# Kernel optimization log

Measured on AMD Instinct MI355X. Metric: run time of the kernel, lower is better.

The kernel has to match this reference:

```python
import jax, jax.numpy as jnp
import numpy as np

DIM = 1024
HEADS = 16
HEAD_DIM = DIM // HEADS
SCALE = HEAD_DIM ** -0.5


def setup_inputs() -> dict:
    key = jax.random.key(0)
    k1, k2, k3, k4 = jax.random.split(key, 4)
    x = jax.random.normal(k1, (8, 1024, DIM), dtype=jnp.float32)
    # nn.Linear weight is [out, in]; init ~ small values
    W_qkv = jax.random.normal(k2, (3 * DIM, DIM), dtype=jnp.float32) * 0.02
    W_proj = jax.random.normal(k3, (DIM, DIM), dtype=jnp.float32) * 0.02
    b_proj = jax.random.normal(k4, (DIM,), dtype=jnp.float32) * 0.02
    return {"x": x, "W_qkv": W_qkv, "W_proj": W_proj, "b_proj": b_proj}


def reference(x, W_qkv, W_proj, b_proj):
    b, n, _ = x.shape
    h, d = HEADS, HEAD_DIM
    qkv = x @ W_qkv.T  # [b, n, 3*dim]
    # rearrange 'b n (qkv h d) -> qkv b h n d'
    qkv = qkv.reshape(b, n, 3, h, d).transpose(2, 0, 3, 1, 4)
    q, k, v = qkv[0], qkv[1], qkv[2]  # each [b, h, n, d]
    dots = jnp.einsum('bhid,bhjd->bhij', q, k) * SCALE
    attn = jax.nn.softmax(dots, axis=-1)
    out = jnp.einsum('bhij,bhjd->bhid', attn, v)
    out = out.transpose(0, 2, 1, 3).reshape(b, n, h * d)  # b n (h d)
    return out @ W_proj.T + b_proj
```

## Files before the change

kernel.cpp:

```cpp
#include <hip/hip_runtime.h>
#include <math.h>

#define DIM   1024
#define HEADS 16
#define HDIM  64
#define SEQ   1024
#define BATCH 8
#define QSCALE 0.1803368801111204f
#define LDH   72
#define ABM   128

typedef __attribute__((ext_vector_type(8))) short          short8_t;
typedef __attribute__((ext_vector_type(8))) unsigned short ushort8_t;
typedef __attribute__((ext_vector_type(4))) unsigned short ushort4_t;
typedef __attribute__((ext_vector_type(4))) float          floatx4;

__device__ __forceinline__ unsigned short f2bf(float f) {
    unsigned u = __float_as_uint(f);
    u += 0x7fffu + ((u >> 16) & 1u);
    return (unsigned short)(u >> 16);
}
__device__ __forceinline__ unsigned rnd_bf(float f) {
    unsigned u = __float_as_uint(f);
    return u + 0x7fffu + ((u >> 16) & 1u);
}
__device__ __forceinline__ float fast_exp2(float x) {
#if __has_builtin(__builtin_amdgcn_exp2f)
    return __builtin_amdgcn_exp2f(x);
#else
    return exp2f(x);
#endif
}
__device__ __forceinline__ void glds16(const unsigned short* g, unsigned short* l) {
    __builtin_amdgcn_global_load_lds(
        (const __attribute__((address_space(1))) void*)g,
        (__attribute__((address_space(3))) void*)l, 16, 0, 0);
}

__global__ __launch_bounds__(256) void cvt_bf16_all(const float* __restrict__ x,
                                                    const float* __restrict__ wqkv,
                                                    const float* __restrict__ wproj,
                                                    unsigned short* __restrict__ x_o,
                                                    unsigned short* __restrict__ wqkv_o,
                                                    unsigned short* __restrict__ wproj_o) {
    const int N8_X = BATCH * SEQ * DIM / 8;
    const int N8_WQ = 3 * DIM * DIM / 8;
    const int N8_WP = DIM * DIM / 8;
    int i = blockIdx.x * 256 + threadIdx.x;
    const float* in;
    unsigned short* out;
    if (i < N8_X)               { in = x;     out = x_o; }
    else if (i < N8_X + N8_WQ)  { i -= N8_X;  in = wqkv; out = wqkv_o; }
    else                        { i -= N8_X + N8_WQ;
                                  if (i >= N8_WP) return;
                                  in = wproj; out = wproj_o; }
    const float4* p = (const float4*)in + (size_t)i * 2;
    float4 a = p[0], b = p[1];
    ushort8_t u;
    u[0] = f2bf(a.x); u[1] = f2bf(a.y); u[2] = f2bf(a.z); u[3] = f2bf(a.w);
    u[4] = f2bf(b.x); u[5] = f2bf(b.y); u[6] = f2bf(b.z); u[7] = f2bf(b.w);
    ((ushort8_t*)out)[i] = u;
}

template<int MODE>
__global__ __launch_bounds__(256) void gemm_nt_mfma(const unsigned short* __restrict__ A,
                                                    const unsigned short* __restrict__ B,
                                                    const float* __restrict__ bias,
                                                    void* __restrict__ Cout,
                                                    unsigned short* __restrict__ vt,
                                                    int M, int N, int K) {
    __shared__ __align__(16) unsigned short As[128 * 64];
    __shared__ __align__(16) unsigned short Bs[128 * 64];

    const int tid  = threadIdx.x;
    const int lane = tid & 63;
    const int wave = tid >> 6;
    const int wm = (wave >> 1) * 64;
    const int wn = (wave & 1) * 64;
    const size_t brow = (size_t)blockIdx.y * 128;
    const size_t bcol = (size_t)blockIdx.x * 128;

    const int srow   = lane >> 3;
    const int schunk = (lane & 7) ^ srow;
    const unsigned short* gA = A + (brow + wave * 8 + srow) * (size_t)K + schunk * 8;
    const unsigned short* gB = B + (bcol + wave * 8 + srow) * (size_t)K + schunk * 8;
    unsigned short* lA = &As[wave * 512 + lane * 8];
    unsigned short* lB = &Bs[wave * 512 + lane * 8];

    floatx4 acc[4][4];
    #pragma unroll
    for (int i = 0; i < 4; i++)
        #pragma unroll
        for (int j = 0; j < 4; j++) acc[i][j] = (floatx4){0.f, 0.f, 0.f, 0.f};

    const int g  = lane >> 4;
    const int rr = lane & 15;
    const int xr = rr & 7;

    for (int k0 = 0; k0 < K; k0 += 64) {
        __syncthreads();
        #pragma unroll
        for (int r = 0; r < 4; r++) {
            glds16(gA + (size_t)r * 32 * K + k0, lA + r * 2048);
            glds16(gB + (size_t)r * 32 * K + k0, lB + r * 2048);
        }
        __syncthreads();

        #pragma unroll
        for (int kc = 0; kc < 2; kc++) {
            const int ch = ((kc * 4 + g) ^ xr) * 8;
            short8_t af[4], bfr[4];
            #pragma unroll
            for (int mi = 0; mi < 4; mi++)
                af[mi] = *(const short8_t*)&As[(wm + mi * 16 + rr) * 64 + ch];
            #pragma unroll
            for (int ni = 0; ni < 4; ni++)
                bfr[ni] = *(const short8_t*)&Bs[(wn + ni * 16 + rr) * 64 + ch];
            #pragma unroll
            for (int mi = 0; mi < 4; mi++)
                #pragma unroll
                for (int ni = 0; ni < 4; ni++)
                    acc[mi][ni] = __builtin_amdgcn_mfma_f32_16x16x32_bf16(
                        af[mi], bfr[ni], acc[mi][ni], 0, 0, 0);
        }
    }

    const int crow = (lane >> 4) * 4;
    const int ccol = lane & 15;

    if (MODE == 0) {
        #pragma unroll
        for (int mi = 0; mi < 4; mi++)
            #pragma unroll
            for (int ni = 0; ni < 4; ni++) {
                const size_t col = bcol + wn + ni * 16 + ccol;
                const float bv = bias[col];
                #pragma unroll
                for (int r = 0; r < 4; r++) {
                    const size_t row = brow + wm + mi * 16 + crow + r;
                    ((float*)Cout)[row * N + col] = acc[mi][ni][r] + bv;
                }
            }
    } else {
        if (bcol < 2048) {
            const float sc = (bcol < 1024) ? QSCALE : 1.0f;
            unsigned short* qk = (unsigned short*)Cout;
            #pragma unroll
            for (int mi = 0; mi < 4; mi++)
                #pragma unroll
                for (int ni = 0; ni < 4; ni++) {
                    const size_t col = bcol + wn + ni * 16 + ccol;
                    #pragma unroll
                    for (int r = 0; r < 4; r++) {
                        const size_t row = brow + wm + mi * 16 + crow + r;
                        qk[row * 2048 + col] = f2bf(acc[mi][ni][r] * sc);
                    }
                }
        } else {
            #pragma unroll
            for (int mi = 0; mi < 4; mi++)
                #pragma unroll
                for (int ni = 0; ni < 4; ni++) {
                    const int dall = (int)(bcol + wn + ni * 16 + ccol) - 2048;
                    const int h = dall >> 6, d = dall & 63;
                    const size_t row0 = brow + wm + mi * 16 + crow;
                    const size_t bb = row0 >> 10;
                    const int n0 = (int)(row0 & 1023);
                    ushort4_t o;
                    #pragma unroll
                    for (int r = 0; r < 4; r++) o[r] = f2bf(acc[mi][ni][r]);
                    *(ushort4_t*)&vt[(((size_t)bb * HEADS + h) * HDIM + d) * SEQ + n0] = o;
                }
        }
    }
}

__global__ __launch_bounds__(256) void attn_mfma(const unsigned short* __restrict__ qk,
                                                 const unsigned short* __restrict__ vt,
                                                 unsigned short* __restrict__ aout) {
    const int qt = blockIdx.x;
    const int h  = blockIdx.y;
    const int b  = blockIdx.z;
    const int tid  = threadIdx.x;
    const int lane = tid & 63;
    const int wave = tid >> 6;
    const int g = lane >> 4;
    const int c = lane & 15;

    __shared__ __align__(16) unsigned short Qs[ABM * LDH];
    __shared__ __align__(16) unsigned short Ks[64 * LDH];
    __shared__ __align__(16) unsigned short Vs[64 * LDH];
    __shared__ float scr[4][2][16];

    const int sr = tid >> 2;
    const int sq = tid & 3;
    const unsigned short* ksrc0 =
        qk + ((size_t)(b * SEQ + sr)) * 2048 + DIM + h * HDIM + sq * 16;
    const unsigned short* vsrc0 =
        vt + (((size_t)(b * HEADS + h)) * HDIM + sr) * SEQ + sq * 16;

    ushort8_t ck0 = *(const ushort8_t*)ksrc0;
    ushort8_t ck1 = *(const ushort8_t*)(ksrc0 + 8);
    ushort8_t cv0 = *(const ushort8_t*)vsrc0;
    ushort8_t cv1 = *(const ushort8_t*)(vsrc0 + 8);

    {
        const int r  = tid >> 1;
        const int c0 = (tid & 1) * 32;
        const unsigned short* src =
            qk + ((size_t)(b * SEQ + qt * ABM + r)) * 2048 + h * HDIM + c0;
        unsigned short* dst = &Qs[r * LDH + c0];
        *(ushort8_t*)(dst)      = *(const ushort8_t*)(src);
        *(ushort8_t*)(dst + 8)  = *(const ushort8_t*)(src + 8);
        *(ushort8_t*)(dst + 16) = *(const ushort8_t*)(src + 16);
        *(ushort8_t*)(dst + 24) = *(const ushort8_t*)(src + 24);
    }
    __syncthreads();

    short8_t bq[2][2];
    #pragma unroll
    for (int f = 0; f < 2; f++)
        #pragma unroll
        for (int kc = 0; kc < 2; kc++)
            bq[f][kc] = *(const short8_t*)&Qs[(f * 64 + wave * 16 + c) * LDH + g * 8 + kc * 32];

    floatx4 O[2][4];
    #pragma unroll
    for (int f = 0; f < 2; f++)
        #pragma unroll
        for (int i = 0; i < 4; i++) O[f][i] = (floatx4){0.f, 0.f, 0.f, 0.f};
    float lsum[2] = {0.f, 0.f};

    for (int kt = 0; kt < SEQ / 64; kt++) {
        ushort8_t nk0, nk1, nv0, nv1;
        if (kt + 1 < SEQ / 64) {
            const unsigned short* ks = ksrc0 + (size_t)(kt + 1) * 64 * 2048;
            const unsigned short* vs = vsrc0 + (kt + 1) * 64;
            nk0 = *(const ushort8_t*)ks;
            nk1 = *(const ushort8_t*)(ks + 8);
            nv0 = *(const ushort8_t*)vs;
            nv1 = *(const ushort8_t*)(vs + 8);
        }
        __syncthreads();
        *(ushort8_t*)&Ks[sr * LDH + sq * 16]     = ck0;
        *(ushort8_t*)&Ks[sr * LDH + sq * 16 + 8] = ck1;
        *(ushort8_t*)&Vs[sr * LDH + sq * 16]     = cv0;
        *(ushort8_t*)&Vs[sr * LDH + sq * 16 + 8] = cv1;
        __syncthreads();

        short8_t ak[4][2];
        #pragma unroll
        for (int nt = 0; nt < 4; nt++)
            #pragma unroll
            for (int kc = 0; kc < 2; kc++)
                ak[nt][kc] = *(const short8_t*)&Ks[(nt * 16 + c) * LDH + g * 8 + kc * 32];

        floatx4 S[2][4];
        #pragma unroll
        for (int f = 0; f < 2; f++)
            #pragma unroll
            for (int nt = 0; nt < 4; nt++) S[f][nt] = (floatx4){0.f, 0.f, 0.f, 0.f};
        #pragma unroll
        for (int f = 0; f < 2; f++)
            #pragma unroll
            for (int nt = 0; nt < 4; nt++)
                #pragma unroll
                for (int kc = 0; kc < 2; kc++)
                    S[f][nt] = __builtin_amdgcn_mfma_f32_16x16x32_bf16(
                        ak[nt][kc], bq[f][kc], S[f][nt], 0, 0, 0);

        #pragma unroll
        for (int f = 0; f < 2; f++)
            #pragma unroll
            for (int nt = 0; nt < 4; nt++) {
                const float p0 = fast_exp2(S[f][nt][0]);
                const float p1 = fast_exp2(S[f][nt][1]);
                const float p2 = fast_exp2(S[f][nt][2]);
                const float p3 = fast_exp2(S[f][nt][3]);
                lsum[f] += (p0 + p1) + (p2 + p3);
                const unsigned r01 = __builtin_amdgcn_perm(rnd_bf(p1), rnd_bf(p0), 0x07060302);
                const unsigned r23 = __builtin_amdgcn_perm(rnd_bf(p3), rnd_bf(p2), 0x07060302);
                *(uint2*)&Qs[(f * 64 + wave * 16 + c) * LDH + nt * 16 + g * 4] =
                    make_uint2(r01, r23);
            }

        short8_t bv[4][2];
        #pragma unroll
        for (int dnt = 0; dnt < 4; dnt++)
            #pragma unroll
            for (int kc = 0; kc < 2; kc++)
                bv[dnt][kc] = *(const short8_t*)&Vs[(dnt * 16 + c) * LDH + g * 8 + kc * 32];

        #pragma unroll
        for (int f = 0; f < 2; f++) {
            short8_t ap[2];
            #pragma unroll
            for (int kc = 0; kc < 2; kc++)
                ap[kc] = *(const short8_t*)&Qs[(f * 64 + wave * 16 + c) * LDH + g * 8 + kc * 32];
            #pragma unroll
            for (int dnt = 0; dnt < 4; dnt++)
                #pragma unroll
                for (int kc = 0; kc < 2; kc++)
                    O[f][dnt] = __builtin_amdgcn_mfma_f32_16x16x32_bf16(
                        ap[kc], bv[dnt][kc], O[f][dnt], 0, 0, 0);
        }

        ck0 = nk0; ck1 = nk1; cv0 = nv0; cv1 = nv1;
    }

    #pragma unroll
    for (int f = 0; f < 2; f++) {
        float s = lsum[f];
        s += __shfl_xor(s, 16);
        s += __shfl_xor(s, 32);
        if (g == 0) scr[wave][f][c] = 1.0f / s;
    }
    __builtin_amdgcn_s_waitcnt(0);

    #pragma unroll
    for (int f = 0; f < 2; f++) {
        const float4 inv4 = *(const float4*)&scr[wave][f][g * 4];
        #pragma unroll
        for (int r = 0; r < 4; r++) {
            const float invl = ((const float*)&inv4)[r];
            const size_t row = (size_t)b * SEQ + qt * ABM + f * 64 + wave * 16 + g * 4 + r;
            #pragma unroll
            for (int dnt = 0; dnt < 4; dnt++)
                aout[row * DIM + h * HDIM + dnt * 16 + c] = f2bf(O[f][dnt][r] * invl);
        }
    }
}

extern "C" void kernel_launch(void* const* d_in, const int* in_sizes, int n_in,
                              void* d_out, int out_size, void* d_ws, size_t ws_size,
                              hipStream_t stream) {
    const float* x      = (const float*)d_in[0];
    const float* W_qkv  = (const float*)d_in[1];
    const float* W_proj = (const float*)d_in[2];
    const float* b_proj = (const float*)d_in[3];
    float* out = (float*)d_out;

    const int M = BATCH * SEQ;

    unsigned short* ws       = (unsigned short*)d_ws;
    unsigned short* x_bf     = ws;
    unsigned short* wqkv_bf  = x_bf + (size_t)M * DIM;
    unsigned short* wproj_bf = wqkv_bf + (size_t)3 * DIM * DIM;
    unsigned short* qk_bf    = wproj_bf + (size_t)DIM * DIM;
    unsigned short* vt_bf    = qk_bf + (size_t)M * 2048;
    unsigned short* aout_bf  = vt_bf + (size_t)BATCH * HEADS * HDIM * SEQ;

    {
        const int n8 = (M * DIM + 3 * DIM * DIM + DIM * DIM) / 8;
        cvt_bf16_all<<<(n8 + 255) / 256, 256, 0, stream>>>(
            x, W_qkv, W_proj, x_bf, wqkv_bf, wproj_bf);
    }

    gemm_nt_mfma<2><<<dim3(3 * DIM / 128, M / 128), 256, 0, stream>>>(
        x_bf, wqkv_bf, nullptr, qk_bf, vt_bf, M, 3 * DIM, DIM);

    attn_mfma<<<dim3(SEQ / ABM, HEADS, BATCH), 256, 0, stream>>>(qk_bf, vt_bf, aout_bf);

    gemm_nt_mfma<0><<<dim3(DIM / 128, M / 128), 256, 0, stream>>>(
        aout_bf, wproj_bf, b_proj, out, nullptr, M, DIM, DIM);
}
```

Measured before the change: 244.4 us.

## Double-buffer K/V tiles with XOR swizzle and reorder block grid mapping

The attention kernel now keeps two K/V shared-memory buffers, indexed by iteration parity. This removes one of the two barriers per key tile, so each tile's stores can overlap the previous tile's compute. K/V rows drop the padded 72 stride for a 64-wide layout with an XOR chunk swizzle to avoid bank conflicts. Grid dimensions for both GEMMs and the attention kernel are also swapped: M-tiles and batch-head pairs go on blockIdx.x, which changes L2 reuse of weight columns and K/V across concurrently running blocks. Shared memory use grows and the single-barrier scheme relies on the parity buffer for correctness.

New measurement: 232.2 us. 5.0% less time.

```diff
diff --git a/kernel.cpp b/kernel.cpp
--- a/kernel.cpp
+++ b/kernel.cpp
@@ -77,8 +77,8 @@
     const int wave = tid >> 6;
     const int wm = (wave >> 1) * 64;
     const int wn = (wave & 1) * 64;
-    const size_t brow = (size_t)blockIdx.y * 128;
-    const size_t bcol = (size_t)blockIdx.x * 128;
+    const size_t brow = (size_t)blockIdx.x * 128;
+    const size_t bcol = (size_t)blockIdx.y * 128;
 
     const int srow   = lane >> 3;
     const int schunk = (lane & 7) ^ srow;
@@ -178,9 +178,10 @@
 __global__ __launch_bounds__(256) void attn_mfma(const unsigned short* __restrict__ qk,
                                                  const unsigned short* __restrict__ vt,
                                                  unsigned short* __restrict__ aout) {
-    const int qt = blockIdx.x;
-    const int h  = blockIdx.y;
-    const int b  = blockIdx.z;
+    const int bh = blockIdx.x;
+    const int qt = blockIdx.y;
+    const int h  = bh & 15;
+    const int b  = bh >> 4;
     const int tid  = threadIdx.x;
     const int lane = tid & 63;
     const int wave = tid >> 6;
@@ -188,16 +189,19 @@
     const int c = lane & 15;
 
     __shared__ __align__(16) unsigned short Qs[ABM * LDH];
-    __shared__ __align__(16) unsigned short Ks[64 * LDH];
-    __shared__ __align__(16) unsigned short Vs[64 * LDH];
+    __shared__ __align__(16) unsigned short Ks[2][64 * 64];
+    __shared__ __align__(16) unsigned short Vs[2][64 * 64];
     __shared__ float scr[4][2][16];
 
     const int sr = tid >> 2;
     const int sq = tid & 3;
+    const int sx = sr & 7;
     const unsigned short* ksrc0 =
         qk + ((size_t)(b * SEQ + sr)) * 2048 + DIM + h * HDIM + sq * 16;
     const unsigned short* vsrc0 =
         vt + (((size_t)(b * HEADS + h)) * HDIM + sr) * SEQ + sq * 16;
+    const int kvo0 = sr * 64 + (((sq * 2)     ^ sx) * 8);
+    const int kvo1 = sr * 64 + (((sq * 2 + 1) ^ sx) * 8);
 
     ushort8_t ck0 = *(const ushort8_t*)ksrc0;
     ushort8_t ck1 = *(const ushort8_t*)(ksrc0 + 8);
@@ -231,29 +235,31 @@
         for (int i = 0; i < 4; i++) O[f][i] = (floatx4){0.f, 0.f, 0.f, 0.f};
     float lsum[2] = {0.f, 0.f};
 
+    const int fro0 = ((0 * 4 + g) ^ (c & 7)) * 8;
+    const int fro1 = ((1 * 4 + g) ^ (c & 7)) * 8;
+
     for (int kt = 0; kt < SEQ / 64; kt++) {
-        ushort8_t nk0, nk1, nv0, nv1;
+        const int cur = kt & 1;
+        *(ushort8_t*)&Ks[cur][kvo0] = ck0;
+        *(ushort8_t*)&Ks[cur][kvo1] = ck1;
+        *(ushort8_t*)&Vs[cur][kvo0] = cv0;
+        *(ushort8_t*)&Vs[cur][kvo1] = cv1;
         if (kt + 1 < SEQ / 64) {
             const unsigned short* ks = ksrc0 + (size_t)(kt + 1) * 64 * 2048;
             const unsigned short* vs = vsrc0 + (kt + 1) * 64;
-            nk0 = *(const ushort8_t*)ks;
-            nk1 = *(const ushort8_t*)(ks + 8);
-            nv0 = *(const ushort8_t*)vs;
-            nv1 = *(const ushort8_t*)(vs + 8);
+            ck0 = *(const ushort8_t*)ks;
+            ck1 = *(const ushort8_t*)(ks + 8);
+            cv0 = *(const ushort8_t*)vs;
+            cv1 = *(const ushort8_t*)(vs + 8);
         }
         __syncthreads();
-        *(ushort8_t*)&Ks[sr * LDH + sq * 16]     = ck0;
-        *(ushort8_t*)&Ks[sr * LDH + sq * 16 + 8] = ck1;
-        *(ushort8_t*)&Vs[sr * LDH + sq * 16]     = cv0;
-        *(ushort8_t*)&Vs[sr * LDH + sq * 16 + 8] = cv1;
-        __syncthreads();
 
         short8_t ak[4][2];
         #pragma unroll
-        for (int nt = 0; nt < 4; nt++)
-            #pragma unroll
-            for (int kc = 0; kc < 2; kc++)
-                ak[nt][kc] = *(const short8_t*)&Ks[(nt * 16 + c) * LDH + g * 8 + kc * 32];
+        for (int nt = 0; nt < 4; nt++) {
+            ak[nt][0] = *(const short8_t*)&Ks[cur][(nt * 16 + c) * 64 + fro0];
+            ak[nt][1] = *(const short8_t*)&Ks[cur][(nt * 16 + c) * 64 + fro1];
+        }
 
         floatx4 S[2][4];
         #pragma unroll
@@ -286,10 +292,10 @@
 
         short8_t bv[4][2];
         #pragma unroll
-        for (int dnt = 0; dnt < 4; dnt++)
-            #pragma unroll
-            for (int kc = 0; kc < 2; kc++)
-                bv[dnt][kc] = *(const short8_t*)&Vs[(dnt * 16 + c) * LDH + g * 8 + kc * 32];
+        for (int dnt = 0; dnt < 4; dnt++) {
+            bv[dnt][0] = *(const short8_t*)&Vs[cur][(dnt * 16 + c) * 64 + fro0];
+            bv[dnt][1] = *(const short8_t*)&Vs[cur][(dnt * 16 + c) * 64 + fro1];
+        }
 
         #pragma unroll
         for (int f = 0; f < 2; f++) {
@@ -304,8 +310,6 @@
                     O[f][dnt] = __builtin_amdgcn_mfma_f32_16x16x32_bf16(
                         ap[kc], bv[dnt][kc], O[f][dnt], 0, 0, 0);
         }
-
-        ck0 = nk0; ck1 = nk1; cv0 = nv0; cv1 = nv1;
     }
 
     #pragma unroll
@@ -356,11 +360,11 @@
             x, W_qkv, W_proj, x_bf, wqkv_bf, wproj_bf);
     }
 
-    gemm_nt_mfma<2><<<dim3(3 * DIM / 128, M / 128), 256, 0, stream>>>(
+    gemm_nt_mfma<2><<<dim3(M / 128, 3 * DIM / 128), 256, 0, stream>>>(
         x_bf, wqkv_bf, nullptr, qk_bf, vt_bf, M, 3 * DIM, DIM);
 
-    attn_mfma<<<dim3(SEQ / ABM, HEADS, BATCH), 256, 0, stream>>>(qk_bf, vt_bf, aout_bf);
-
-    gemm_nt_mfma<0><<<dim3(DIM / 128, M / 128), 256, 0, stream>>>(
+    attn_mfma<<<dim3(BATCH * HEADS, SEQ / ABM), 256, 0, stream>>>(qk_bf, vt_bf, aout_bf);
+
+    gemm_nt_mfma<0><<<dim3(M / 128, DIM / 128), 256, 0, stream>>>(
         aout_bf, wproj_bf, b_proj, out, nullptr, M, DIM, DIM);
 }
```
